# Kernel optimization log

Measured on AMD Instinct MI355X. Metric: run time of the kernel, lower is better.

## Reference

```python
import jax, jax.numpy as jnp
import numpy as np

B, C, R, D = 32, 30, 196, 256
K = 20            # max_det_per_class
CONF = 0.5        # conf_threshold
IOU_THR = 0.3     # iou_threshold


def setup_inputs() -> dict:
    key = jax.random.key(0)
    k1, k2, k3 = jax.random.split(key, 3)
    return {
        "local_features": jax.random.normal(k1, (B, C, R, D), dtype=jnp.float32),
        "W_coords": jax.random.normal(k2, (4, D), dtype=jnp.float32) * 0.02,
        "b_coords": jnp.zeros((4,), jnp.float32),
        "W_pres": jax.random.normal(k3, (1, D), dtype=jnp.float32) * 0.02,
        "b_pres": jnp.zeros((1,), jnp.float32),
    }


def _grid_centers_xyxy(num_regions):
    # centers of a GxG grid in normalized coords, repeated to width 4 (xyxy)
    g = int(round(np.sqrt(num_regions)))
    assert g * g == num_regions
    c = (np.arange(g, dtype=np.float32) + 0.5) / g
    cy, cx = np.meshgrid(c, c, indexing="ij")
    centers = np.stack([cx, cy], axis=-1).reshape(-1, 2)  # [R, 2]
    return jnp.asarray(np.tile(centers, (1, 2)))          # [R, 4]


def _pairwise_iou(boxes):
    # boxes: [K, 4] xyxy -> [K, K]
    x1, y1, x2, y2 = boxes[:, 0], boxes[:, 1], boxes[:, 2], boxes[:, 3]
    area = jnp.clip(x2 - x1, 0) * jnp.clip(y2 - y1, 0)
    xx1 = jnp.maximum(x1[:, None], x1[None, :])
    yy1 = jnp.maximum(y1[:, None], y1[None, :])
    xx2 = jnp.minimum(x2[:, None], x2[None, :])
    yy2 = jnp.minimum(y2[:, None], y2[None, :])
    inter = jnp.clip(xx2 - xx1, 0) * jnp.clip(yy2 - yy1, 0)
    union = area[:, None] + area[None, :] - inter
    return inter / jnp.maximum(union, 1e-9)


def _nms_keep(boxes, valid):
    # boxes: [K, 4] already sorted by descending score; valid: [K] bool
    iou = _pairwise_iou(boxes)
    later = jnp.arange(K)

    def body(i, keep):
        sup = keep[i] & (iou[i] > IOU_THR) & (later > i)
        return keep & (~sup)

    return jax.lax.fori_loop(0, K, body, valid)


def _forward(local_features, W_coords, b_coords, W_pres, b_pres):
    # Linear heads: [B, C, R, D] -> [B, C, R, 4] and [B, C, R, 1]
    coords = jnp.einsum("bcrd,od->bcro", local_features, W_coords) + b_coords
    presence = jnp.einsum("bcrd,od->bcro", local_features, W_pres) + b_pres
    probs = jax.nn.sigmoid(presence[..., 0])  # [B, C, R]

    # predict_relative with xyxy format: add grid centers
    coords = coords + _grid_centers_xyxy(R)[None, None]

    # top-k per (image, class); top_k returns scores sorted descending
    probs_k, idx = jax.lax.top_k(probs, K)                      # [B, C, K]
    coords_k = jnp.take_along_axis(coords, idx[..., None], axis=2)  # [B, C, K, 4]

    # confidence threshold (padded mask instead of dynamic shapes)
    valid = probs_k > CONF

    # per-(image, class) greedy NMS; class shift in original => class-separable
    keep = jax.vmap(jax.vmap(_nms_keep))(coords_k, valid)       # [B, C, K] bool
    kf = keep.astype(coords_k.dtype)
    coords_out = coords_k * kf[..., None]
    probs_out = probs_k * kf
    return coords_out, probs_out, keep, presence


def reference(local_features, W_coords, b_coords, W_pres, b_pres):
    return _forward(local_features, W_coords, b_coords, W_pres, b_pres)
```

## Files before the change

kernel.cpp:

```cpp
#include <hip/hip_runtime.h>
#include <hip/hip_bf16.h>
#include <math.h>

#define BB 32
#define CC 30
#define RR 196
#define DD 256
#define KK 20
#define GG 14
#define CONF_ 0.5f
#define IOU_THR_ 0.3f

constexpr int NROWS = BB * CC * RR;
constexpr int COORDS_OFF = 0;
constexpr int PROBS_OFF  = BB * CC * KK * 4;
constexpr int KEEP_OFF   = PROBS_OFF + BB * CC * KK;
constexpr int PRES_OFF   = KEEP_OFF + BB * CC * KK;

__device__ __forceinline__ float dot4(float4 a, float4 b) {
    return a.x * b.x + a.y * b.y + a.z * b.z + a.w * b.w;
}

__global__ __launch_bounds__(256) void mlp_kernel(
    const float4* __restrict__ lf,
    const float*  __restrict__ W_coords,
    const float*  __restrict__ b_coords,
    const float*  __restrict__ W_pres,
    const float*  __restrict__ b_pres,
    float*  __restrict__ presence_out,
    float4* __restrict__ boxes_ws)
{
    const int lane = threadIdx.x & 63;
    const int wave = blockIdx.x * 4 + (threadIdx.x >> 6);
    const int sub  = lane >> 2;
    const int q    = lane & 3;

    const int row = wave * 16 + sub;
    const float4* __restrict__ rowp = lf + (size_t)row * 64 + q;
    const float4* __restrict__ Wp4  = reinterpret_cast<const float4*>(W_pres) + q;
    const float4* __restrict__ Wc4  = reinterpret_cast<const float4*>(W_coords) + q;

    float ap = 0.f, a0 = 0.f, a1 = 0.f, a2 = 0.f, a3 = 0.f;
    #pragma unroll 4
    for (int t = 0; t < 16; ++t) {
        const float4 x = rowp[4 * t];
        ap += dot4(x, Wp4[4 * t]);
        a0 += dot4(x, Wc4[4 * t]);
        a1 += dot4(x, Wc4[64 + 4 * t]);
        a2 += dot4(x, Wc4[128 + 4 * t]);
        a3 += dot4(x, Wc4[192 + 4 * t]);
    }
    ap += __shfl_xor(ap, 1); ap += __shfl_xor(ap, 2);
    a0 += __shfl_xor(a0, 1); a0 += __shfl_xor(a0, 2);
    a1 += __shfl_xor(a1, 1); a1 += __shfl_xor(a1, 2);
    a2 += __shfl_xor(a2, 1); a2 += __shfl_xor(a2, 2);
    a3 += __shfl_xor(a3, 1); a3 += __shfl_xor(a3, 2);

    if (q == 0) {
        presence_out[row] = ap + b_pres[0];
        const int   r  = row % RR;
        const int   ix = r % GG, iy = r / GG;
        const float cx = (ix + 0.5f) / (float)GG;
        const float cy = (iy + 0.5f) / (float)GG;
        boxes_ws[row] = make_float4(a0 + b_coords[0] + cx,
                                    a1 + b_coords[1] + cy,
                                    a2 + b_coords[2] + cx,
                                    a3 + b_coords[3] + cy);
    }
}

__global__ __launch_bounds__(256) void topk_nms_kernel(
    const float*  __restrict__ presence,
    const float4* __restrict__ boxes_ws,
    const float*  __restrict__ presence_dummy_keepalive,
    float* __restrict__ coords_out,
    float* __restrict__ probs_out,
    float* __restrict__ keep_out)
{
    const int wv   = threadIdx.x >> 6;
    const int lane = threadIdx.x & 63;
    const int bc   = blockIdx.x * 4 + wv;

    const float* pres = presence + (size_t)bc * RR;
    float v[4]; int id[4];
    #pragma unroll
    for (int t = 0; t < 4; ++t) {
        const int r = lane + 64 * t;
        id[t] = r;
        v[t]  = (r < RR) ? pres[r] : -1e30f;
    }

    float myv = -1e30f; int myi = 0;
    for (int k = 0; k < KK; ++k) {
        float bv = v[0]; int bi = id[0];
        #pragma unroll
        for (int t = 1; t < 4; ++t)
            if (v[t] > bv || (v[t] == bv && id[t] < bi)) { bv = v[t]; bi = id[t]; }
        #pragma unroll
        for (int off = 32; off; off >>= 1) {
            const float ov = __shfl_xor(bv, off);
            const int   oi = __shfl_xor(bi, off);
            if (ov > bv || (ov == bv && oi < bi)) { bv = ov; bi = oi; }
        }
        #pragma unroll
        for (int t = 0; t < 4; ++t)
            if (id[t] == bi) v[t] = -1e30f;
        if (lane == k) { myv = bv; myi = bi; }
    }

    float x1 = 0.f, y1 = 0.f, x2 = 0.f, y2 = 0.f, area = 0.f, prob = 0.f;
    int kp = 0;
    if (lane < KK) {
        const float4 b = boxes_ws[(size_t)bc * RR + myi];
        x1 = b.x; y1 = b.y; x2 = b.z; y2 = b.w;
        area = fmaxf(x2 - x1, 0.f) * fmaxf(y2 - y1, 0.f);
        prob = 1.f / (1.f + expf(-myv));
        kp   = (prob > CONF_) ? 1 : 0;
    }
    for (int i = 0; i < KK; ++i) {
        const int   ki  = __shfl(kp, i);
        const float bx1 = __shfl(x1, i), by1 = __shfl(y1, i);
        const float bx2 = __shfl(x2, i), by2 = __shfl(y2, i);
        const float ai  = __shfl(area, i);
        if (lane > i && lane < KK && ki) {
            const float xx1 = fmaxf(x1, bx1), yy1 = fmaxf(y1, by1);
            const float xx2 = fminf(x2, bx2), yy2 = fminf(y2, by2);
            const float inter = fmaxf(xx2 - xx1, 0.f) * fmaxf(yy2 - yy1, 0.f);
            const float uni   = area + ai - inter;
            const float iou   = inter / fmaxf(uni, 1e-9f);
            if (iou > IOU_THR_) kp = 0;
        }
    }

    if (lane < KK) {
        const size_t base = (size_t)bc * KK + lane;
        const float  kf   = kp ? 1.f : 0.f;
        coords_out[base * 4 + 0] = x1 * kf;
        coords_out[base * 4 + 1] = y1 * kf;
        coords_out[base * 4 + 2] = x2 * kf;
        coords_out[base * 4 + 3] = y2 * kf;
        probs_out[base] = prob * kf;
        keep_out[base]  = kf;
    }
}

__global__ __launch_bounds__(64) void topk_nms_recompute_kernel(
    const float4* __restrict__ lf,
    const float*  __restrict__ W_coords,
    const float*  __restrict__ b_coords,
    const float*  __restrict__ presence,
    float* __restrict__ coords_out,
    float* __restrict__ probs_out,
    float* __restrict__ keep_out)
{
    const int bc   = blockIdx.x;
    const int lane = threadIdx.x;

    __shared__ float s_topv[KK];
    __shared__ int   s_topi[KK];
    __shared__ float s_box[KK][4];

    const float* pres = presence + (size_t)bc * RR;
    float v[4]; int id[4];
    #pragma unroll
    for (int t = 0; t < 4; ++t) {
        const int r = lane + 64 * t;
        id[t] = r;
        v[t]  = (r < RR) ? pres[r] : -1e30f;
    }
    for (int k = 0; k < KK; ++k) {
        float bv = v[0]; int bi = id[0];
        #pragma unroll
        for (int t = 1; t < 4; ++t)
            if (v[t] > bv || (v[t] == bv && id[t] < bi)) { bv = v[t]; bi = id[t]; }
        #pragma unroll
        for (int off = 32; off; off >>= 1) {
            const float ov = __shfl_xor(bv, off);
            const int   oi = __shfl_xor(bi, off);
            if (ov > bv || (ov == bv && oi < bi)) { bv = ov; bi = oi; }
        }
        #pragma unroll
        for (int t = 0; t < 4; ++t)
            if (id[t] == bi) v[t] = -1e30f;
        if (lane == 0) { s_topv[k] = bv; s_topi[k] = bi; }
    }
    __syncthreads();

    const int g  = lane >> 4;
    const int sl = lane & 15;
    float4 wc[4][4];
    #pragma unroll
    for (int o = 0; o < 4; ++o)
        #pragma unroll
        for (int t = 0; t < 4; ++t)
            wc[o][t] = reinterpret_cast<const float4*>(W_coords + o * DD)[sl + 16 * t];

    #pragma unroll
    for (int it = 0; it < KK / 4; ++it) {
        const int k   = it * 4 + g;
        const int row = s_topi[k];
        const float4* __restrict__ rp = lf + ((size_t)bc * RR + row) * 64 + sl;
        float acc[4] = {0.f, 0.f, 0.f, 0.f};
        #pragma unroll
        for (int t = 0; t < 4; ++t) {
            const float4 x = rp[16 * t];
            #pragma unroll
            for (int o = 0; o < 4; ++o)
                acc[o] += x.x * wc[o][t].x + x.y * wc[o][t].y
                        + x.z * wc[o][t].z + x.w * wc[o][t].w;
        }
        #pragma unroll
        for (int off = 8; off; off >>= 1) {
            #pragma unroll
            for (int o = 0; o < 4; ++o) acc[o] += __shfl_xor(acc[o], off);
        }
        if (sl == 0) {
            const int   ix = row % GG, iy = row / GG;
            const float cx = (ix + 0.5f) / (float)GG;
            const float cy = (iy + 0.5f) / (float)GG;
            s_box[k][0] = acc[0] + b_coords[0] + cx;
            s_box[k][1] = acc[1] + b_coords[1] + cy;
            s_box[k][2] = acc[2] + b_coords[2] + cx;
            s_box[k][3] = acc[3] + b_coords[3] + cy;
        }
    }
    __syncthreads();

    float x1 = 0.f, y1 = 0.f, x2 = 0.f, y2 = 0.f, area = 0.f, prob = 0.f;
    int kp = 0;
    if (lane < KK) {
        x1 = s_box[lane][0]; y1 = s_box[lane][1];
        x2 = s_box[lane][2]; y2 = s_box[lane][3];
        area = fmaxf(x2 - x1, 0.f) * fmaxf(y2 - y1, 0.f);
        prob = 1.f / (1.f + expf(-s_topv[lane]));
        kp = (prob > CONF_) ? 1 : 0;
    }
    for (int i = 0; i < KK; ++i) {
        const int   ki  = __shfl(kp, i);
        const float bx1 = __shfl(x1, i), by1 = __shfl(y1, i);
        const float bx2 = __shfl(x2, i), by2 = __shfl(y2, i);
        const float ai  = __shfl(area, i);
        if (lane > i && lane < KK && ki) {
            const float xx1 = fmaxf(x1, bx1), yy1 = fmaxf(y1, by1);
            const float xx2 = fminf(x2, bx2), yy2 = fminf(y2, by2);
            const float inter = fmaxf(xx2 - xx1, 0.f) * fmaxf(yy2 - yy1, 0.f);
            const float uni   = area + ai - inter;
            const float iou   = inter / fmaxf(uni, 1e-9f);
            if (iou > IOU_THR_) kp = 0;
        }
    }
    if (lane < KK) {
        const size_t base = (size_t)bc * KK + lane;
        const float  kf   = kp ? 1.f : 0.f;
        coords_out[base * 4 + 0] = x1 * kf;
        coords_out[base * 4 + 1] = y1 * kf;
        coords_out[base * 4 + 2] = x2 * kf;
        coords_out[base * 4 + 3] = y2 * kf;
        probs_out[base] = prob * kf;
        keep_out[base]  = kf;
    }
}

__global__ __launch_bounds__(256) void presence_only_kernel(
    const float4* __restrict__ lf,
    const float*  __restrict__ W_pres,
    const float*  __restrict__ b_pres,
    float* __restrict__ presence_out)
{
    const int lane = threadIdx.x & 63;
    const int wave = blockIdx.x * 4 + (threadIdx.x >> 6);
    const int sub  = lane >> 2;
    const int q    = lane & 3;
    const int row  = wave * 16 + sub;
    const float4* __restrict__ rowp = lf + (size_t)row * 64 + q;
    const float4* __restrict__ wp   = reinterpret_cast<const float4*>(W_pres) + q;

    float p = 0.f;
    #pragma unroll
    for (int t = 0; t < 16; ++t) {
        const float4 x = rowp[4 * t];
        const float4 w = wp[4 * t];
        p += dot4(x, w);
    }
    p += __shfl_xor(p, 1);
    p += __shfl_xor(p, 2);
    if (q == 0) presence_out[row] = p + b_pres[0];
}

extern "C" void kernel_launch(void* const* d_in, const int* in_sizes, int n_in,
                              void* d_out, int out_size, void* d_ws, size_t ws_size,
                              hipStream_t stream) {
    const float* lf       = (const float*)d_in[0];
    const float* W_coords = (const float*)d_in[1];
    const float* b_coords = (const float*)d_in[2];
    const float* W_pres   = (const float*)d_in[3];
    const float* b_pres   = (const float*)d_in[4];

    float* out          = (float*)d_out;
    float* coords_out   = out + COORDS_OFF;
    float* probs_out    = out + PROBS_OFF;
    float* keep_out     = out + KEEP_OFF;
    float* presence_out = out + PRES_OFF;

    const size_t ws_needed = (size_t)NROWS * 4 * sizeof(float);

    if (ws_size >= ws_needed) {
        float4* boxes_ws = (float4*)d_ws;
        mlp_kernel<<<NROWS / 64, 256, 0, stream>>>(
            (const float4*)lf, W_coords, b_coords, W_pres, b_pres,
            presence_out, boxes_ws);
        topk_nms_kernel<<<BB * CC / 4, 256, 0, stream>>>(
            presence_out, boxes_ws, presence_out,
            coords_out, probs_out, keep_out);
    } else {
        presence_only_kernel<<<NROWS / 64, 256, 0, stream>>>(
            (const float4*)lf, W_pres, b_pres, presence_out);
        topk_nms_recompute_kernel<<<BB * CC, 64, 0, stream>>>(
            (const float4*)lf, W_coords, b_coords, presence_out,
            coords_out, probs_out, keep_out);
    }
}
```

Baseline: 57.21 us.

## Make MLP head kernel persistent with register-cached weights and 16-lane row split

The main MLP kernel becomes a grid-stride persistent kernel of 2048 blocks. Each thread loads its slice of the presence and coordinate weights into registers once and reuses them across many rows. Each 16-lane group handles one row with contiguous float4 loads and a 4-step shuffle reduction, where before 4 lanes per row re-read the weights every iteration. This aims to cut repeated weight loads and improve coalescing on a bandwidth-bound read of the features, at the cost of more registers and longer shuffle reductions. The recompute kernel is only moved and an unused argument is removed.

New measurement: 51.46 us. -10.0%, faster.

```diff
diff --git a/kernel.cpp b/kernel.cpp
--- a/kernel.cpp
+++ b/kernel.cpp
@@ -21,7 +21,7 @@
     return a.x * b.x + a.y * b.y + a.z * b.z + a.w * b.w;
 }
 
-__global__ __launch_bounds__(256) void mlp_kernel(
+__global__ __launch_bounds__(256, 4) void mlp_kernel(
     const float4* __restrict__ lf,
     const float*  __restrict__ W_coords,
     const float*  __restrict__ b_coords,
@@ -32,47 +32,65 @@
 {
     const int lane = threadIdx.x & 63;
     const int wave = blockIdx.x * 4 + (threadIdx.x >> 6);
-    const int sub  = lane >> 2;
-    const int q    = lane & 3;
-
-    const int row = wave * 16 + sub;
-    const float4* __restrict__ rowp = lf + (size_t)row * 64 + q;
-    const float4* __restrict__ Wp4  = reinterpret_cast<const float4*>(W_pres) + q;
-    const float4* __restrict__ Wc4  = reinterpret_cast<const float4*>(W_coords) + q;
-
-    float ap = 0.f, a0 = 0.f, a1 = 0.f, a2 = 0.f, a3 = 0.f;
-    #pragma unroll 4
-    for (int t = 0; t < 16; ++t) {
-        const float4 x = rowp[4 * t];
-        ap += dot4(x, Wp4[4 * t]);
-        a0 += dot4(x, Wc4[4 * t]);
-        a1 += dot4(x, Wc4[64 + 4 * t]);
-        a2 += dot4(x, Wc4[128 + 4 * t]);
-        a3 += dot4(x, Wc4[192 + 4 * t]);
-    }
-    ap += __shfl_xor(ap, 1); ap += __shfl_xor(ap, 2);
-    a0 += __shfl_xor(a0, 1); a0 += __shfl_xor(a0, 2);
-    a1 += __shfl_xor(a1, 1); a1 += __shfl_xor(a1, 2);
-    a2 += __shfl_xor(a2, 1); a2 += __shfl_xor(a2, 2);
-    a3 += __shfl_xor(a3, 1); a3 += __shfl_xor(a3, 2);
-
-    if (q == 0) {
-        presence_out[row] = ap + b_pres[0];
-        const int   r  = row % RR;
-        const int   ix = r % GG, iy = r / GG;
-        const float cx = (ix + 0.5f) / (float)GG;
-        const float cy = (iy + 0.5f) / (float)GG;
-        boxes_ws[row] = make_float4(a0 + b_coords[0] + cx,
-                                    a1 + b_coords[1] + cy,
-                                    a2 + b_coords[2] + cx,
-                                    a3 + b_coords[3] + cy);
+    const int gr   = lane >> 4;
+    const int o    = lane & 15;
+
+    const float4* __restrict__ Wp4 = reinterpret_cast<const float4*>(W_pres);
+    const float4* __restrict__ Wc4 = reinterpret_cast<const float4*>(W_coords);
+
+    float4 wp[4], w0[4], w1[4], w2[4], w3[4];
+    #pragma unroll
+    for (int t = 0; t < 4; ++t) {
+        wp[t] = Wp4[o + 16 * t];
+        w0[t] = Wc4[      o + 16 * t];
+        w1[t] = Wc4[ 64 + o + 16 * t];
+        w2[t] = Wc4[128 + o + 16 * t];
+        w3[t] = Wc4[192 + o + 16 * t];
+    }
+    const float bp  = b_pres[0];
+    const float bc0 = b_coords[0], bc1 = b_coords[1];
+    const float bc2 = b_coords[2], bc3 = b_coords[3];
+
+    constexpr int NGRAN = NROWS / 4;
+    const int nwave = 2048 * 4;
+
+    for (int g = wave; g < NGRAN; g += nwave) {
+        const int row = g * 4 + gr;
+        const float4* __restrict__ rp = lf + (size_t)row * 64;
+
+        float ap = 0.f, a0 = 0.f, a1 = 0.f, a2 = 0.f, a3 = 0.f;
+        #pragma unroll
+        for (int t = 0; t < 4; ++t) {
+            const float4 x = rp[o + 16 * t];
+            ap += dot4(x, wp[t]);
+            a0 += dot4(x, w0[t]);
+            a1 += dot4(x, w1[t]);
+            a2 += dot4(x, w2[t]);
+            a3 += dot4(x, w3[t]);
+        }
+        #pragma unroll
+        for (int off = 1; off < 16; off <<= 1) {
+            ap += __shfl_xor(ap, off);
+            a0 += __shfl_xor(a0, off);
+            a1 += __shfl_xor(a1, off);
+            a2 += __shfl_xor(a2, off);
+            a3 += __shfl_xor(a3, off);
+        }
+        if (o == 0) {
+            presence_out[row] = ap + bp;
+            const int   r  = row % RR;
+            const int   ix = r % GG, iy = r / GG;
+            const float cx = (ix + 0.5f) / (float)GG;
+            const float cy = (iy + 0.5f) / (float)GG;
+            boxes_ws[row] = make_float4(a0 + bc0 + cx, a1 + bc1 + cy,
+                                        a2 + bc2 + cx, a3 + bc3 + cy);
+        }
     }
 }
 
 __global__ __launch_bounds__(256) void topk_nms_kernel(
     const float*  __restrict__ presence,
     const float4* __restrict__ boxes_ws,
-    const float*  __restrict__ presence_dummy_keepalive,
     float* __restrict__ coords_out,
     float* __restrict__ probs_out,
     float* __restrict__ keep_out)
@@ -132,123 +150,6 @@
         }
     }
 
-    if (lane < KK) {
-        const size_t base = (size_t)bc * KK + lane;
-        const float  kf   = kp ? 1.f : 0.f;
-        coords_out[base * 4 + 0] = x1 * kf;
-        coords_out[base * 4 + 1] = y1 * kf;
-        coords_out[base * 4 + 2] = x2 * kf;
-        coords_out[base * 4 + 3] = y2 * kf;
-        probs_out[base] = prob * kf;
-        keep_out[base]  = kf;
-    }
-}
-
-__global__ __launch_bounds__(64) void topk_nms_recompute_kernel(
-    const float4* __restrict__ lf,
-    const float*  __restrict__ W_coords,
-    const float*  __restrict__ b_coords,
-    const float*  __restrict__ presence,
-    float* __restrict__ coords_out,
-    float* __restrict__ probs_out,
-    float* __restrict__ keep_out)
-{
-    const int bc   = blockIdx.x;
-    const int lane = threadIdx.x;
-
-    __shared__ float s_topv[KK];
-    __shared__ int   s_topi[KK];
-    __shared__ float s_box[KK][4];
-
-    const float* pres = presence + (size_t)bc * RR;
-    float v[4]; int id[4];
-    #pragma unroll
-    for (int t = 0; t < 4; ++t) {
-        const int r = lane + 64 * t;
-        id[t] = r;
-        v[t]  = (r < RR) ? pres[r] : -1e30f;
-    }
-    for (int k = 0; k < KK; ++k) {
-        float bv = v[0]; int bi = id[0];
-        #pragma unroll
-        for (int t = 1; t < 4; ++t)
-            if (v[t] > bv || (v[t] == bv && id[t] < bi)) { bv = v[t]; bi = id[t]; }
-        #pragma unroll
-        for (int off = 32; off; off >>= 1) {
-            const float ov = __shfl_xor(bv, off);
-            const int   oi = __shfl_xor(bi, off);
-            if (ov > bv || (ov == bv && oi < bi)) { bv = ov; bi = oi; }
-        }
-        #pragma unroll
-        for (int t = 0; t < 4; ++t)
-            if (id[t] == bi) v[t] = -1e30f;
-        if (lane == 0) { s_topv[k] = bv; s_topi[k] = bi; }
-    }
-    __syncthreads();
-
-    const int g  = lane >> 4;
-    const int sl = lane & 15;
-    float4 wc[4][4];
-    #pragma unroll
-    for (int o = 0; o < 4; ++o)
-        #pragma unroll
-        for (int t = 0; t < 4; ++t)
-            wc[o][t] = reinterpret_cast<const float4*>(W_coords + o * DD)[sl + 16 * t];
-
-    #pragma unroll
-    for (int it = 0; it < KK / 4; ++it) {
-        const int k   = it * 4 + g;
-        const int row = s_topi[k];
-        const float4* __restrict__ rp = lf + ((size_t)bc * RR + row) * 64 + sl;
-        float acc[4] = {0.f, 0.f, 0.f, 0.f};
-        #pragma unroll
-        for (int t = 0; t < 4; ++t) {
-            const float4 x = rp[16 * t];
-            #pragma unroll
-            for (int o = 0; o < 4; ++o)
-                acc[o] += x.x * wc[o][t].x + x.y * wc[o][t].y
-                        + x.z * wc[o][t].z + x.w * wc[o][t].w;
-        }
-        #pragma unroll
-        for (int off = 8; off; off >>= 1) {
-            #pragma unroll
-            for (int o = 0; o < 4; ++o) acc[o] += __shfl_xor(acc[o], off);
-        }
-        if (sl == 0) {
-            const int   ix = row % GG, iy = row / GG;
-            const float cx = (ix + 0.5f) / (float)GG;
-            const float cy = (iy + 0.5f) / (float)GG;
-            s_box[k][0] = acc[0] + b_coords[0] + cx;
-            s_box[k][1] = acc[1] + b_coords[1] + cy;
-            s_box[k][2] = acc[2] + b_coords[2] + cx;
-            s_box[k][3] = acc[3] + b_coords[3] + cy;
-        }
-    }
-    __syncthreads();
-
-    float x1 = 0.f, y1 = 0.f, x2 = 0.f, y2 = 0.f, area = 0.f, prob = 0.f;
-    int kp = 0;
-    if (lane < KK) {
-        x1 = s_box[lane][0]; y1 = s_box[lane][1];
-        x2 = s_box[lane][2]; y2 = s_box[lane][3];
-        area = fmaxf(x2 - x1, 0.f) * fmaxf(y2 - y1, 0.f);
-        prob = 1.f / (1.f + expf(-s_topv[lane]));
-        kp = (prob > CONF_) ? 1 : 0;
-    }
-    for (int i = 0; i < KK; ++i) {
-        const int   ki  = __shfl(kp, i);
-        const float bx1 = __shfl(x1, i), by1 = __shfl(y1, i);
-        const float bx2 = __shfl(x2, i), by2 = __shfl(y2, i);
-        const float ai  = __shfl(area, i);
-        if (lane > i && lane < KK && ki) {
-            const float xx1 = fmaxf(x1, bx1), yy1 = fmaxf(y1, by1);
-            const float xx2 = fminf(x2, bx2), yy2 = fminf(y2, by2);
-            const float inter = fmaxf(xx2 - xx1, 0.f) * fmaxf(yy2 - yy1, 0.f);
-            const float uni   = area + ai - inter;
-            const float iou   = inter / fmaxf(uni, 1e-9f);
-            if (iou > IOU_THR_) kp = 0;
-        }
-    }
     if (lane < KK) {
         const size_t base = (size_t)bc * KK + lane;
         const float  kf   = kp ? 1.f : 0.f;
@@ -277,14 +178,127 @@
 
     float p = 0.f;
     #pragma unroll
-    for (int t = 0; t < 16; ++t) {
-        const float4 x = rowp[4 * t];
-        const float4 w = wp[4 * t];
-        p += dot4(x, w);
-    }
+    for (int t = 0; t < 16; ++t) p += dot4(rowp[4 * t], wp[4 * t]);
     p += __shfl_xor(p, 1);
     p += __shfl_xor(p, 2);
     if (q == 0) presence_out[row] = p + b_pres[0];
+}
+
+__global__ __launch_bounds__(64) void topk_nms_recompute_kernel(
+    const float4* __restrict__ lf,
+    const float*  __restrict__ W_coords,
+    const float*  __restrict__ b_coords,
+    const float*  __restrict__ presence,
+    float* __restrict__ coords_out,
+    float* __restrict__ probs_out,
+    float* __restrict__ keep_out)
+{
+    const int bc   = blockIdx.x;
+    const int lane = threadIdx.x;
+
+    __shared__ float s_topv[KK];
+    __shared__ int   s_topi[KK];
+    __shared__ float s_box[KK][4];
+
+    const float* pres = presence + (size_t)bc * RR;
+    float v[4]; int id[4];
+    #pragma unroll
+    for (int t = 0; t < 4; ++t) {
+        const int r = lane + 64 * t;
+        id[t] = r;
+        v[t]  = (r < RR) ? pres[r] : -1e30f;
+    }
+    for (int k = 0; k < KK; ++k) {
+        float bv = v[0]; int bi = id[0];
+        #pragma unroll
+        for (int t = 1; t < 4; ++t)
+            if (v[t] > bv || (v[t] == bv && id[t] < bi)) { bv = v[t]; bi = id[t]; }
+        #pragma unroll
+        for (int off = 32; off; off >>= 1) {
+            const float ov = __shfl_xor(bv, off);
+            const int   oi = __shfl_xor(bi, off);
+            if (ov > bv || (ov == bv && oi < bi)) { bv = ov; bi = oi; }
+        }
+        #pragma unroll
+        for (int t = 0; t < 4; ++t)
+            if (id[t] == bi) v[t] = -1e30f;
+        if (lane == 0) { s_topv[k] = bv; s_topi[k] = bi; }
+    }
+    __syncthreads();
+
+    const int g  = lane >> 4;
+    const int sl = lane & 15;
+    float4 wc[4][4];
+    #pragma unroll
+    for (int o = 0; o < 4; ++o)
+        #pragma unroll
+        for (int t = 0; t < 4; ++t)
+            wc[o][t] = reinterpret_cast<const float4*>(W_coords + o * DD)[sl + 16 * t];
+
+    #pragma unroll
+    for (int it = 0; it < KK / 4; ++it) {
+        const int k   = it * 4 + g;
+        const int row = s_topi[k];
+        const float4* __restrict__ rp = lf + ((size_t)bc * RR + row) * 64 + sl;
+        float acc[4] = {0.f, 0.f, 0.f, 0.f};
+        #pragma unroll
+        for (int t = 0; t < 4; ++t) {
+            const float4 x = rp[16 * t];
+            #pragma unroll
+            for (int o = 0; o < 4; ++o)
+                acc[o] += x.x * wc[o][t].x + x.y * wc[o][t].y
+                        + x.z * wc[o][t].z + x.w * wc[o][t].w;
+        }
+        #pragma unroll
+        for (int off = 8; off; off >>= 1) {
+            #pragma unroll
+            for (int o = 0; o < 4; ++o) acc[o] += __shfl_xor(acc[o], off);
+        }
+        if (sl == 0) {
+            const int   ix = row % GG, iy = row / GG;
+            const float cx = (ix + 0.5f) / (float)GG;
+            const float cy = (iy + 0.5f) / (float)GG;
+            s_box[k][0] = acc[0] + b_coords[0] + cx;
+            s_box[k][1] = acc[1] + b_coords[1] + cy;
+            s_box[k][2] = acc[2] + b_coords[2] + cx;
+            s_box[k][3] = acc[3] + b_coords[3] + cy;
+        }
+    }
+    __syncthreads();
+
+    float x1 = 0.f, y1 = 0.f, x2 = 0.f, y2 = 0.f, area = 0.f, prob = 0.f;
+    int kp = 0;
+    if (lane < KK) {
+        x1 = s_box[lane][0]; y1 = s_box[lane][1];
+        x2 = s_box[lane][2]; y2 = s_box[lane][3];
+        area = fmaxf(x2 - x1, 0.f) * fmaxf(y2 - y1, 0.f);
+        prob = 1.f / (1.f + expf(-s_topv[lane]));
+        kp = (prob > CONF_) ? 1 : 0;
+    }
+    for (int i = 0; i < KK; ++i) {
+        const int   ki  = __shfl(kp, i);
+        const float bx1 = __shfl(x1, i), by1 = __shfl(y1, i);
+        const float bx2 = __shfl(x2, i), by2 = __shfl(y2, i);
+        const float ai  = __shfl(area, i);
+        if (lane > i && lane < KK && ki) {
+            const float xx1 = fmaxf(x1, bx1), yy1 = fmaxf(y1, by1);
+            const float xx2 = fminf(x2, bx2), yy2 = fminf(y2, by2);
+            const float inter = fmaxf(xx2 - xx1, 0.f) * fmaxf(yy2 - yy1, 0.f);
+            const float uni   = area + ai - inter;
+            const float iou   = inter / fmaxf(uni, 1e-9f);
+            if (iou > IOU_THR_) kp = 0;
+        }
+    }
+    if (lane < KK) {
+        const size_t base = (size_t)bc * KK + lane;
+        const float  kf   = kp ? 1.f : 0.f;
+        coords_out[base * 4 + 0] = x1 * kf;
+        coords_out[base * 4 + 1] = y1 * kf;
+        coords_out[base * 4 + 2] = x2 * kf;
+        coords_out[base * 4 + 3] = y2 * kf;
+        probs_out[base] = prob * kf;
+        keep_out[base]  = kf;
+    }
 }
 
 extern "C" void kernel_launch(void* const* d_in, const int* in_sizes, int n_in,
@@ -306,11 +320,11 @@
 
     if (ws_size >= ws_needed) {
         float4* boxes_ws = (float4*)d_ws;
-        mlp_kernel<<<NROWS / 64, 256, 0, stream>>>(
+        mlp_kernel<<<2048, 256, 0, stream>>>(
             (const float4*)lf, W_coords, b_coords, W_pres, b_pres,
             presence_out, boxes_ws);
         topk_nms_kernel<<<BB * CC / 4, 256, 0, stream>>>(
-            presence_out, boxes_ws, presence_out,
+            presence_out, boxes_ws,
             coords_out, probs_out, keep_out);
     } else {
         presence_only_kernel<<<NROWS / 64, 256, 0, stream>>>(
```
